# Kernel optimization log

Measured on AMD Instinct MI355X. Metric: run time of the kernel, lower is better.

## Reference

```python
import jax, jax.numpy as jnp
import numpy as np

N = 100000     # nodes
E = 1600000    # edges (avg degree 16)
CI = 3         # input features (x, z, t)
W = 128        # hidden width
CO = 1         # output features
L = 4          # processor layers


def setup_inputs() -> dict:
    key = jax.random.key(0)
    ks = jax.random.split(key, 10)
    s = 0.1
    x = jax.random.normal(ks[0], (N, CI), jnp.float32)
    # compute_mask is an external geometry-dependent, no-grad mask; emulate as 0/1 node mask
    mask = (jax.random.uniform(ks[1], (N, 1)) > 0.5).astype(jnp.float32)
    edge_index = jax.random.randint(ks[2], (2, E), 0, N, dtype=jnp.int32)
    W_enc = jax.random.normal(ks[3], (CI, W), jnp.float32) * s
    b_enc = jnp.zeros((W,), jnp.float32)
    W_p = jax.random.normal(ks[4], (L, W, W), jnp.float32) * s
    b_p = jnp.zeros((L, W), jnp.float32)
    W_dec = jax.random.normal(ks[5], (W, CO), jnp.float32) * s
    b_dec = jnp.zeros((CO,), jnp.float32)
    return {"x": x, "mask": mask, "edge_index": edge_index,
            "W_enc": W_enc, "b_enc": b_enc, "W_p": W_p, "b_p": b_p,
            "W_dec": W_dec, "b_dec": b_dec}


def reference(x, mask, edge_index, W_enc, b_enc, W_p, b_p, W_dec, b_dec):
    src, dst = edge_index[0], edge_index[1]
    n = x.shape[0]
    # GCN symmetric normalization with self-loops: deg = 1 + in-degree
    deg = 1.0 + jax.ops.segment_sum(jnp.ones((src.shape[0],), x.dtype), dst, num_segments=n)
    dis = jax.lax.rsqrt(deg)                      # deg^{-1/2}, [N]
    norm = dis[src] * dis[dst]                    # [E]

    def gcn(h, Wt, b):
        h = h @ Wt                                # [N, out]
        agg = jax.ops.segment_sum(h[src] * norm[:, None], dst, num_segments=n)
        # self-loop contribution: norm_ii = dis_i^2
        return agg + h * (dis * dis)[:, None] + b

    h = jax.nn.relu(gcn(x, W_enc, b_enc))
    for l in range(L):
        h = jax.nn.relu(gcn(h, W_p[l], b_p[l]))
    out = gcn(h, W_dec, b_dec)
    return out * mask
```

## Files before the change

### kernel.cpp

```cpp
#include <hip/hip_runtime.h>
#include <hip/hip_fp16.h>


#define HW 128
#define NBMAX 1024
#define CAP 4096
#define PBLK 256
#define GBR 256

typedef _Float16 f16x8 __attribute__((ext_vector_type(8)));
typedef float f32x4 __attribute__((ext_vector_type(4)));

__global__ void k_zero_i32(int* __restrict__ a, int n) {
    int i = blockIdx.x * 256 + threadIdx.x;
    if (i < n) a[i] = 0;
}

__global__ __launch_bounds__(256) void k_histb(const int* __restrict__ dstA,
                                               int* __restrict__ bcnt,
                                               int* __restrict__ pcnt,
                                               int nb, int e, int nblk) {
    __shared__ int lh[NBMAX];
    for (int b = threadIdx.x; b < nb; b += 256) lh[b] = 0;
    __syncthreads();
    int blk = blockIdx.x;
    int c0 = (int)(((long long)e * blk) / nblk);
    int c1 = (int)(((long long)e * (blk + 1)) / nblk);
    for (int i = c0 + threadIdx.x; i < c1; i += 256) atomicAdd(&lh[dstA[i] >> 7], 1);
    __syncthreads();
    for (int b = threadIdx.x; b < nb; b += 256) {
        int v = lh[b];
        pcnt[(size_t)blk * nb + b] = v;
        if (v) atomicAdd(&bcnt[b], v);
    }
}

__global__ void k_bscan(const int* __restrict__ bcnt, int* __restrict__ bstart,
                        int nb, int etot) {
    __shared__ int s[1024];
    int t = threadIdx.x;
    int d0 = (t < nb) ? bcnt[t] : 0;
    s[t] = d0;
    __syncthreads();
    for (int off = 1; off < 1024; off <<= 1) {
        int v = (t >= off) ? s[t - off] : 0;
        __syncthreads();
        s[t] += v;
        __syncthreads();
    }
    if (t < nb) bstart[t] = s[t] - d0;
    if (t == 0) bstart[nb] = etot;
}

__global__ __launch_bounds__(PBLK) void k_soff2(const int* __restrict__ pcnt,
                                                const int* __restrict__ bstart,
                                                int* __restrict__ soff, int nb) {
    __shared__ int s[PBLK];
    int b = blockIdx.x, t = threadIdx.x;
    int v = pcnt[(size_t)t * nb + b];
    s[t] = v;
    __syncthreads();
    for (int off = 1; off < PBLK; off <<= 1) {
        int u = (t >= off) ? s[t - off] : 0;
        __syncthreads();
        s[t] += u;
        __syncthreads();
    }
    soff[(size_t)t * nb + b] = bstart[b] + s[t] - v;
}

__global__ __launch_bounds__(256) void k_part(const int* __restrict__ srcA,
                                              const int* __restrict__ dstA,
                                              const int* __restrict__ soff,
                                              unsigned* __restrict__ stage,
                                              int nb, int e, int nblk) {
    __shared__ int loff[NBMAX];
    __shared__ int lh[NBMAX];
    int blk = blockIdx.x;
    for (int b = threadIdx.x; b < nb; b += 256) {
        loff[b] = soff[(size_t)blk * nb + b];
        lh[b] = 0;
    }
    __syncthreads();
    int c0 = (int)(((long long)e * blk) / nblk);
    int c1 = (int)(((long long)e * (blk + 1)) / nblk);
    for (int i = c0 + threadIdx.x; i < c1; i += 256) {
        int d = dstA[i];
        int bk = d >> 7;
        int p = loff[bk] + atomicAdd(&lh[bk], 1);
        stage[p] = ((unsigned)srcA[i] << 7) | (unsigned)(d & 127);
    }
}

__global__ __launch_bounds__(256) void k_build(const unsigned* __restrict__ stage,
                                               const int* __restrict__ bstart,
                                               const float* __restrict__ x,
                                               int* __restrict__ row_start,
                                               float* __restrict__ dis,
                                               float4* __restrict__ x4,
                                               int* __restrict__ csr, int n, int nb) {
    __shared__ int lcnt[128];
    __shared__ int sc[128];
    __shared__ int lcsr[CAP];
    int b = blockIdx.x, tid = threadIdx.x;
    int base = bstart[b], end = bstart[b + 1], cnt = end - base;
    int node0 = b << 7;

    if (tid < 128) lcnt[tid] = 0;
    __syncthreads();
    for (int j = tid; j < cnt; j += 256) atomicAdd(&lcnt[stage[base + j] & 127], 1);
    __syncthreads();
    if (tid < 128) sc[tid] = lcnt[tid];
    __syncthreads();
    for (int off = 1; off < 128; off <<= 1) {
        int v = (tid < 128 && tid >= off) ? sc[tid - off] : 0;
        __syncthreads();
        if (tid < 128) sc[tid] += v;
        __syncthreads();
    }
    int node = node0 + tid;
    if (tid < 128 && node < n) {
        int excl = sc[tid] - lcnt[tid];
        row_start[node] = base + excl;
        float dv = rsqrtf(1.f + (float)lcnt[tid]);
        dis[node] = dv;
        x4[node] = make_float4(x[node * 3] * dv, x[node * 3 + 1] * dv,
                               x[node * 3 + 2] * dv, 0.f);
    }
    if (tid == 0 && b == nb - 1) row_start[n] = end;
    __syncthreads();
    if (tid < 128) sc[tid] = sc[tid] - lcnt[tid];
    if (tid < 128) lcnt[tid] = 0;
    __syncthreads();
    if (cnt <= CAP) {
        for (int j = tid; j < cnt; j += 256) {
            unsigned v = stage[base + j];
            int dl = v & 127;
            int p = atomicAdd(&lcnt[dl], 1);
            lcsr[sc[dl] + p] = (int)(v >> 7);
        }
        __syncthreads();
        for (int j = tid; j < cnt; j += 256) csr[base + j] = lcsr[j];
    } else {
        for (int j = tid; j < cnt; j += 256) {
            unsigned v = stage[base + j];
            int dl = v & 127;
            int p = atomicAdd(&lcnt[dl], 1);
            csr[base + sc[dl] + p] = (int)(v >> 7);
        }
    }
}

__global__ void k_prep_wt(const float* __restrict__ Wp, __half* __restrict__ WTh,
                          __half* __restrict__ WTl, int total) {
    int t = blockIdx.x * 256 + threadIdx.x;
    if (t >= total) return;
    int l = t >> 14;
    int kc = t & 16383;
    int k = kc >> 7, c = kc & 127;
    float w = Wp[t];
    __half hi = __float2half_rn(w);
    __half lo = __float2half_rn(w - __half2float(hi));
    size_t o = ((size_t)l << 14) + (size_t)c * HW + k;
    WTh[o] = hi;
    WTl[o] = lo;
}

__global__ void k_enc_agg(const float4* __restrict__ x4, const int* __restrict__ rs,
                          const int* __restrict__ csr, const float* __restrict__ dis,
                          float4* __restrict__ zx, int n) {
    int i = blockIdx.x * 256 + threadIdx.x;
    if (i >= n) return;
    float4 a = x4[i];
    int e1 = rs[i + 1];
    for (int j = rs[i]; j < e1; ++j) {
        float4 v = x4[csr[j]];
        a.x += v.x; a.y += v.y; a.z += v.z;
    }
    float d = dis[i];
    zx[i] = make_float4(a.x * d, a.y * d, a.z * d, 0.f);
}

__global__ void k_enc_gemm(const float4* __restrict__ zx, const float* __restrict__ We,
                           const float* __restrict__ be, const float* __restrict__ dis,
                           __half* __restrict__ H, int n) {
    int t = blockIdx.x * 256 + threadIdx.x;
    int i = t >> 7;
    int c = t & 127;
    if (i >= n) return;
    float4 z = zx[i];
    float v = z.x * We[c] + z.y * We[HW + c] + z.z * We[2 * HW + c] + be[c];
    H[(size_t)i * HW + c] = __float2half_rn(fmaxf(v, 0.f) * dis[i]);
}

__global__ __launch_bounds__(256) void k_agg128(const __half* __restrict__ Hin,
                                                const int* __restrict__ rs,
                                                const int* __restrict__ csr,
                                                const float* __restrict__ dis,
                                                __half* __restrict__ Z, int n) {
    int wave = threadIdx.x >> 6, lane = threadIdx.x & 63;
    int lg = lane & 15;
    int node = (blockIdx.x * 4 + wave) * 4 + (lane >> 4);
    bool active = node < n;

    float a0[8], a1[8], a2[8], a3[8];
#pragma unroll
    for (int j = 0; j < 8; ++j) { a0[j] = 0.f; a1[j] = 0.f; a2[j] = 0.f; a3[j] = 0.f; }

    int e0 = 0, e1 = 0;
    if (active) {
        e0 = rs[node];
        e1 = rs[node + 1];
        f16x8 hv = *(const f16x8*)(Hin + (size_t)node * HW + lg * 8);
#pragma unroll
        for (int j = 0; j < 8; ++j) a0[j] = (float)hv[j];
    }

    for (int base = e0; base < e1; base += 16) {
        int cnt = e1 - base;
        if (cnt > 16) cnt = 16;
        int sl = (base + lg < e1) ? csr[base + lg] : 0;
        int k = 0;
        for (; k + 4 <= cnt; k += 4) {
            int s0 = __shfl(sl, k + 0, 16);
            int s1 = __shfl(sl, k + 1, 16);
            int s2 = __shfl(sl, k + 2, 16);
            int s3 = __shfl(sl, k + 3, 16);
            f16x8 v0 = *(const f16x8*)(Hin + (size_t)s0 * HW + lg * 8);
            f16x8 v1 = *(const f16x8*)(Hin + (size_t)s1 * HW + lg * 8);
            f16x8 v2 = *(const f16x8*)(Hin + (size_t)s2 * HW + lg * 8);
            f16x8 v3 = *(const f16x8*)(Hin + (size_t)s3 * HW + lg * 8);
#pragma unroll
            for (int j = 0; j < 8; ++j) {
                a0[j] += (float)v0[j];
                a1[j] += (float)v1[j];
                a2[j] += (float)v2[j];
                a3[j] += (float)v3[j];
            }
        }
        for (; k < cnt; ++k) {
            int s = __shfl(sl, k, 16);
            f16x8 v = *(const f16x8*)(Hin + (size_t)s * HW + lg * 8);
#pragma unroll
            for (int j = 0; j < 8; ++j) a0[j] += (float)v[j];
        }
    }

    if (active) {
        float d = dis[node];
        union { uint4 u; __half2 h[4]; } pk;
#pragma unroll
        for (int j = 0; j < 4; ++j) {
            float lo = d * ((a0[2 * j] + a1[2 * j]) + (a2[2 * j] + a3[2 * j]));
            float hi = d * ((a0[2 * j + 1] + a1[2 * j + 1]) + (a2[2 * j + 1] + a3[2 * j + 1]));
            pk.h[j] = __floats2half2_rn(lo, hi);
        }
        *(uint4*)(Z + (size_t)node * HW + lg * 8) = pk.u;
    }
}

__global__ __launch_bounds__(256) void k_gemmw(const __half* __restrict__ Z,
                                               const __half* __restrict__ WTh,
                                               const __half* __restrict__ WTl,
                                               const float* __restrict__ b,
                                               const float* __restrict__ dis,
                                               __half* __restrict__ Hout,
                                               const float* __restrict__ Wd,
                                               float* __restrict__ tout,
                                               int mode, int n) {
    __shared__ __half ws[2][128][128];
    int tid = threadIdx.x;
    int wave = tid >> 6, lane = tid & 63;
    int q = lane >> 4, r16 = lane & 15;

#pragma unroll
    for (int p = 0; p < 16; ++p) {
        int idx = p * 256 + tid;
        int slot = idx & 15;
        int col = (idx >> 4) & 127;
        int hl = idx >> 11;
        const __half* src = hl ? WTl : WTh;
        f16x8 v = *(const f16x8*)(src + (size_t)col * HW + slot * 8);
        *(f16x8*)(&ws[hl][col][(slot ^ (col & 7)) * 8]) = v;
    }
    __syncthreads();

    for (int rt = 0; rt < GBR / 64; ++rt) {
        int row0 = blockIdx.x * GBR + rt * 64 + wave * 16;
        if (row0 >= n) break;

        f16x8 afr[4];
#pragma unroll
        for (int ks = 0; ks < 4; ++ks) {
            int row = row0 + r16;
            row = row < n ? row : (n - 1);
            afr[ks] = *(const f16x8*)(Z + (size_t)row * HW + ks * 32 + q * 8);
        }

        f32x4 acc[8];
#pragma unroll
        for (int nt = 0; nt < 8; ++nt) acc[nt] = (f32x4)0.f;
#pragma unroll
        for (int ks = 0; ks < 4; ++ks) {
            int sslot = ((ks * 4 + q) ^ (r16 & 7)) * 8;
#pragma unroll
            for (int nt = 0; nt < 8; ++nt) {
                int col = nt * 16 + r16;
                f16x8 bh = *(const f16x8*)(&ws[0][col][sslot]);
                f16x8 bl = *(const f16x8*)(&ws[1][col][sslot]);
                acc[nt] = __builtin_amdgcn_mfma_f32_16x16x32_f16(afr[ks], bh, acc[nt], 0, 0, 0);
                acc[nt] = __builtin_amdgcn_mfma_f32_16x16x32_f16(afr[ks], bl, acc[nt], 0, 0, 0);
            }
        }

        if (mode == 0) {
#pragma unroll
            for (int nt = 0; nt < 8; ++nt) {
                int col = nt * 16 + r16;
                float bias = b[col];
#pragma unroll
                for (int r = 0; r < 4; ++r) {
                    int row = row0 + q * 4 + r;
                    if (row < n) {
                        float v = fmaxf(acc[nt][r] + bias, 0.f) * dis[row];
                        Hout[(size_t)row * HW + col] = __float2half_rn(v);
                    }
                }
            }
        } else {
            float pr[4] = {0.f, 0.f, 0.f, 0.f};
#pragma unroll
            for (int nt = 0; nt < 8; ++nt) {
                int col = nt * 16 + r16;
                float bias = b[col];
                float wd = Wd[col];
#pragma unroll
                for (int r = 0; r < 4; ++r)
                    pr[r] += fmaxf(acc[nt][r] + bias, 0.f) * wd;
            }
#pragma unroll
            for (int r = 0; r < 4; ++r) {
#pragma unroll
                for (int off = 1; off < 16; off <<= 1) pr[r] += __shfl_xor(pr[r], off, 16);
                if (r16 == 0) {
                    int row = row0 + q * 4 + r;
                    if (row < n) tout[row] = pr[r] * dis[row];
                }
            }
        }
    }
}

__global__ void k_dec_out(const float* __restrict__ t, const int* __restrict__ rs,
                          const int* __restrict__ csr, const float* __restrict__ dis,
                          const float* __restrict__ bdec, const float* __restrict__ mask,
                          float* __restrict__ out, int n) {
    int i = blockIdx.x * 256 + threadIdx.x;
    if (i >= n) return;
    float acc = t[i];
    int e1 = rs[i + 1];
    for (int j = rs[i]; j < e1; ++j) acc += t[csr[j]];
    out[i] = (dis[i] * acc + bdec[0]) * mask[i];
}

static inline size_t align256(size_t x) { return (x + 255) & ~(size_t)255; }

extern "C" void kernel_launch(void* const* d_in, const int* in_sizes, int n_in,
                              void* d_out, int out_size, void* d_ws, size_t ws_size,
                              hipStream_t stream) {
    const float* x     = (const float*)d_in[0];
    const float* mask  = (const float*)d_in[1];
    const int*   ei    = (const int*)d_in[2];
    const float* W_enc = (const float*)d_in[3];
    const float* b_enc = (const float*)d_in[4];
    const float* W_p   = (const float*)d_in[5];
    const float* b_p   = (const float*)d_in[6];
    const float* W_dec = (const float*)d_in[7];
    const float* b_dec = (const float*)d_in[8];

    const int N = in_sizes[1];
    const int E = in_sizes[2] / 2;
    const int* srcA = ei;
    const int* dstA = ei + E;
    const int NB = (N + 127) >> 7;

    char* p = (char*)d_ws;
    size_t off = 0;
    auto carve = [&](size_t bytes) {
        void* r = p + off;
        off += align256(bytes);
        return r;
    };
    int*      bcnt      = (int*)carve((size_t)NB * 4);
    int*      bstart    = (int*)carve((size_t)(NB + 1) * 4);
    int*      pcnt      = (int*)carve((size_t)PBLK * NB * 4);
    int*      soff      = (int*)carve((size_t)PBLK * NB * 4);
    int*      row_start = (int*)carve((size_t)(N + 1) * 4);
    unsigned* stage     = (unsigned*)carve((size_t)E * 4);
    int*      csr       = (int*)carve((size_t)E * 4);
    float*    dis       = (float*)carve((size_t)N * 4);
    float4*   x4        = (float4*)carve((size_t)N * 16);
    float4*   zx        = (float4*)carve((size_t)N * 16);
    float*    tdec      = (float*)carve((size_t)N * 4);
    __half*   WTh       = (__half*)carve((size_t)4 * HW * HW * 2);
    __half*   WTl       = (__half*)carve((size_t)4 * HW * HW * 2);
    __half*   HA        = (__half*)carve((size_t)N * HW * 2);
    __half*   HB        = (__half*)carve((size_t)N * HW * 2);

    const int gN   = (N + 255) / 256;
    const int gAgg = (N + 15) / 16;
    const int gG   = (N + GBR - 1) / GBR;
    const int WPT  = 4 * HW * HW;

    k_zero_i32<<<(NB + 255) / 256, 256, 0, stream>>>(bcnt, NB);
    k_histb<<<PBLK, 256, 0, stream>>>(dstA, bcnt, pcnt, NB, E, PBLK);
    k_bscan<<<1, 1024, 0, stream>>>(bcnt, bstart, NB, E);
    k_soff2<<<NB, PBLK, 0, stream>>>(pcnt, bstart, soff, NB);
    k_part<<<PBLK, 256, 0, stream>>>(srcA, dstA, soff, stage, NB, E, PBLK);
    k_build<<<NB, 256, 0, stream>>>(stage, bstart, x, row_start, dis, x4, csr, N, NB);
    k_prep_wt<<<(WPT + 255) / 256, 256, 0, stream>>>(W_p, WTh, WTl, WPT);

    k_enc_agg<<<gN, 256, 0, stream>>>(x4, row_start, csr, dis, zx, N);
    k_enc_gemm<<<(N * HW + 255) / 256, 256, 0, stream>>>(zx, W_enc, b_enc, dis, HA, N);

    __half* Hin = HA;
    __half* Hoth = HB;
    for (int l = 0; l < 4; ++l) {
        k_agg128<<<gAgg, 256, 0, stream>>>(Hin, row_start, csr, dis, Hoth, N);
        int mode = (l == 3) ? 1 : 0;
        k_gemmw<<<gG, 256, 0, stream>>>(Hoth, WTh + (size_t)l * HW * HW,
                                        WTl + (size_t)l * HW * HW,
                                        b_p + (size_t)l * HW, dis, Hoth,
                                        W_dec, tdec, mode, N);
        __half* t = Hin; Hin = Hoth; Hoth = t;
    }

    k_dec_out<<<gN, 256, 0, stream>>>(tdec, row_start, csr, dis, b_dec, mask,
                                      (float*)d_out, N);
}
```

Baseline: 471.3 us.

## Split hidden features into two 64-column slabs for cache-friendlier aggregation

Stores the fp16 hidden state as two column slabs of 64 features each, so each slab is N x 64 and half the size of the full matrix. The aggregation kernel now processes one slab per block, with 8 lanes per node instead of 16, and interleaves slab blocks so that neighbouring blocks work on the same slab. The encoder, GEMM load and GEMM store paths are changed to read and write the slab layout. The aim is to raise cache hit rates on the random neighbour gathers. In exchange, each CSR row is read twice and the GEMM epilogue stores become more scattered.

New measurement: 463.1 us (median of 2 runs). No clear change (-1.7%).

```diff
diff --git a/kernel.cpp b/kernel.cpp
--- a/kernel.cpp
+++ b/kernel.cpp
@@ -190,18 +190,22 @@
     if (i >= n) return;
     float4 z = zx[i];
     float v = z.x * We[c] + z.y * We[HW + c] + z.z * We[2 * HW + c] + be[c];
-    H[(size_t)i * HW + c] = __float2half_rn(fmaxf(v, 0.f) * dis[i]);
-}
-
-__global__ __launch_bounds__(256) void k_agg128(const __half* __restrict__ Hin,
+    H[((size_t)(c >> 6) * n + i) * 64 + (c & 63)] = __float2half_rn(fmaxf(v, 0.f) * dis[i]);
+}
+
+__global__ __launch_bounds__(256) void k_agg_s2(const __half* __restrict__ Hin,
                                                 const int* __restrict__ rs,
                                                 const int* __restrict__ csr,
                                                 const float* __restrict__ dis,
                                                 __half* __restrict__ Z, int n) {
+    int b = blockIdx.x;
+    int chunk = (b >> 3) * 4 + (b & 3);
+    int s = (b >> 2) & 1;
     int wave = threadIdx.x >> 6, lane = threadIdx.x & 63;
-    int lg = lane & 15;
-    int node = (blockIdx.x * 4 + wave) * 4 + (lane >> 4);
+    int lg = lane & 7;
+    int node = chunk * 32 + wave * 8 + (lane >> 3);
     bool active = node < n;
+    const __half* Hs = Hin + (size_t)s * n * 64;
 
     float a0[8], a1[8], a2[8], a3[8];
 #pragma unroll
@@ -211,25 +215,25 @@
     if (active) {
         e0 = rs[node];
         e1 = rs[node + 1];
-        f16x8 hv = *(const f16x8*)(Hin + (size_t)node * HW + lg * 8);
+        f16x8 hv = *(const f16x8*)(Hs + (size_t)node * 64 + lg * 8);
 #pragma unroll
         for (int j = 0; j < 8; ++j) a0[j] = (float)hv[j];
     }
 
-    for (int base = e0; base < e1; base += 16) {
+    for (int base = e0; base < e1; base += 8) {
         int cnt = e1 - base;
-        if (cnt > 16) cnt = 16;
+        if (cnt > 8) cnt = 8;
         int sl = (base + lg < e1) ? csr[base + lg] : 0;
         int k = 0;
         for (; k + 4 <= cnt; k += 4) {
-            int s0 = __shfl(sl, k + 0, 16);
-            int s1 = __shfl(sl, k + 1, 16);
-            int s2 = __shfl(sl, k + 2, 16);
-            int s3 = __shfl(sl, k + 3, 16);
-            f16x8 v0 = *(const f16x8*)(Hin + (size_t)s0 * HW + lg * 8);
-            f16x8 v1 = *(const f16x8*)(Hin + (size_t)s1 * HW + lg * 8);
-            f16x8 v2 = *(const f16x8*)(Hin + (size_t)s2 * HW + lg * 8);
-            f16x8 v3 = *(const f16x8*)(Hin + (size_t)s3 * HW + lg * 8);
+            int s0 = __shfl(sl, k + 0, 8);
+            int s1 = __shfl(sl, k + 1, 8);
+            int s2 = __shfl(sl, k + 2, 8);
+            int s3 = __shfl(sl, k + 3, 8);
+            f16x8 v0 = *(const f16x8*)(Hs + (size_t)s0 * 64 + lg * 8);
+            f16x8 v1 = *(const f16x8*)(Hs + (size_t)s1 * 64 + lg * 8);
+            f16x8 v2 = *(const f16x8*)(Hs + (size_t)s2 * 64 + lg * 8);
+            f16x8 v3 = *(const f16x8*)(Hs + (size_t)s3 * 64 + lg * 8);
 #pragma unroll
             for (int j = 0; j < 8; ++j) {
                 a0[j] += (float)v0[j];
@@ -239,8 +243,8 @@
             }
         }
         for (; k < cnt; ++k) {
-            int s = __shfl(sl, k, 16);
-            f16x8 v = *(const f16x8*)(Hin + (size_t)s * HW + lg * 8);
+            int sk = __shfl(sl, k, 8);
+            f16x8 v = *(const f16x8*)(Hs + (size_t)sk * 64 + lg * 8);
 #pragma unroll
             for (int j = 0; j < 8; ++j) a0[j] += (float)v[j];
         }
@@ -255,7 +259,7 @@
             float hi = d * ((a0[2 * j + 1] + a1[2 * j + 1]) + (a2[2 * j + 1] + a3[2 * j + 1]));
             pk.h[j] = __floats2half2_rn(lo, hi);
         }
-        *(uint4*)(Z + (size_t)node * HW + lg * 8) = pk.u;
+        *(uint4*)(Z + ((size_t)s * n + node) * 64 + lg * 8) = pk.u;
     }
 }
 
@@ -294,7 +298,8 @@
         for (int ks = 0; ks < 4; ++ks) {
             int row = row0 + r16;
             row = row < n ? row : (n - 1);
-            afr[ks] = *(const f16x8*)(Z + (size_t)row * HW + ks * 32 + q * 8);
+            afr[ks] = *(const f16x8*)(Z + ((size_t)(ks >> 1) * n + row) * 64 +
+                                      (ks & 1) * 32 + q * 8);
         }
 
         f32x4 acc[8];
@@ -317,13 +322,14 @@
 #pragma unroll
             for (int nt = 0; nt < 8; ++nt) {
                 int col = nt * 16 + r16;
+                int cs = col >> 6, c64 = col & 63;
                 float bias = b[col];
 #pragma unroll
                 for (int r = 0; r < 4; ++r) {
                     int row = row0 + q * 4 + r;
                     if (row < n) {
                         float v = fmaxf(acc[nt][r] + bias, 0.f) * dis[row];
-                        Hout[(size_t)row * HW + col] = __float2half_rn(v);
+                        Hout[((size_t)cs * n + row) * 64 + c64] = __float2half_rn(v);
                     }
                 }
             }
@@ -408,7 +414,8 @@
     __half*   HB        = (__half*)carve((size_t)N * HW * 2);
 
     const int gN   = (N + 255) / 256;
-    const int gAgg = (N + 15) / 16;
+    const int nChunk = (N + 31) / 32;
+    const int gAgg = ((nChunk + 3) / 4) * 8;
     const int gG   = (N + GBR - 1) / GBR;
     const int WPT  = 4 * HW * HW;
 
@@ -426,7 +433,7 @@
     __half* Hin = HA;
     __half* Hoth = HB;
     for (int l = 0; l < 4; ++l) {
-        k_agg128<<<gAgg, 256, 0, stream>>>(Hin, row_start, csr, dis, Hoth, N);
+        k_agg_s2<<<gAgg, 256, 0, stream>>>(Hin, row_start, csr, dis, Hoth, N);
         int mode = (l == 3) ? 1 : 0;
         k_gemmw<<<gG, 256, 0, stream>>>(Hoth, WTh + (size_t)l * HW * HW,
                                         WTl + (size_t)l * HW * HW,
```
